# Kernel optimization log

Hardware: AMD Instinct MI355X
Metric: run time of the kernel (lower is better)

## Reference

```python
import jax, jax.numpy as jnp
import numpy as np

B, N, E_PER = 32, 2048, 16384
DIN, H = 128, 128
RATIO = 0.3


def setup_inputs() -> dict:
    key = jax.random.key(0)
    ks = jax.random.split(key, 16)
    s_in = 1.0 / np.sqrt(DIN)
    s_h = 1.0 / np.sqrt(H)
    inp = {
        "x": jax.random.normal(ks[0], (B * N, DIN), dtype=jnp.float32),
        "edge_src": jax.random.randint(ks[1], (B, E_PER), 0, N, dtype=jnp.int32),
        "edge_dst": jax.random.randint(ks[2], (B, E_PER), 0, N, dtype=jnp.int32),
        # SAGEConv layer 1: lin_l (neighbor agg, with bias), lin_r (root, no bias)
        "Wl1": jax.random.normal(ks[3], (H, DIN), dtype=jnp.float32) * s_in,
        "bl1": jnp.zeros((H,), dtype=jnp.float32),
        "Wr1": jax.random.normal(ks[4], (H, DIN), dtype=jnp.float32) * s_in,
        # SAGEConv layer 2
        "Wl2": jax.random.normal(ks[5], (H, H), dtype=jnp.float32) * s_h,
        "bl2": jnp.zeros((H,), dtype=jnp.float32),
        "Wr2": jax.random.normal(ks[6], (H, H), dtype=jnp.float32) * s_h,
        # TopKPooling score weight
        "pool_w": jax.random.normal(ks[7], (H,), dtype=jnp.float32) * s_h,
        # classifier MLP
        "Wc1": jax.random.normal(ks[8], (H, H), dtype=jnp.float32) * s_h,
        "bc1": jnp.zeros((H,), dtype=jnp.float32),
        "Wc2": jax.random.normal(ks[9], (1, H), dtype=jnp.float32) * s_h,
        "bc2": jnp.zeros((1,), dtype=jnp.float32),
    }
    return inp


def _sage_conv(x, src, dst, n_total, Wl, bl, Wr):
    # mean-aggregate neighbor messages: msg flows src -> dst
    msg = x[src]                                                   # [E, D] gather
    agg = jax.ops.segment_sum(msg, dst, num_segments=n_total)      # [Nt, D]
    deg = jax.ops.segment_sum(jnp.ones_like(dst, dtype=x.dtype), dst,
                              num_segments=n_total)
    agg = agg / jnp.maximum(deg, 1.0)[:, None]
    return agg @ Wl.T + bl + x @ Wr.T


def _forward(x, edge_src, edge_dst, Wl1, bl1, Wr1, Wl2, bl2, Wr2,
             pool_w, Wc1, bc1, Wc2, bc2):
    n_total = x.shape[0]
    # offset per-graph node ids into the disjoint-union batch
    off = (jnp.arange(B, dtype=edge_src.dtype) * N)[:, None]
    src = (edge_src + off).reshape(-1)
    dst = (edge_dst + off).reshape(-1)

    x = jax.nn.relu(_sage_conv(x, src, dst, n_total, Wl1, bl1, Wr1))
    x = jax.nn.relu(_sage_conv(x, src, dst, n_total, Wl2, bl2, Wr2))

    # TopKPooling: score = tanh(x . w / ||w||); keep top ceil(ratio*N) per graph
    score = jnp.tanh(x @ pool_w / jnp.linalg.norm(pool_w))         # [Nt]
    k = int(np.ceil(RATIO * N))                                    # 615
    vals, idx = jax.lax.top_k(score.reshape(B, N), k)              # [B, k]
    xg = x.reshape(B, N, -1)
    x_sel = jnp.take_along_axis(xg, idx[..., None], axis=1)        # [B, k, H]
    x_sel = x_sel * vals[..., None]                                # gate by score

    # global mean pool over kept nodes, then MLP classifier
    emb = x_sel.mean(axis=1)                                       # [B, H]
    h = jax.nn.relu(emb @ Wc1.T + bc1)
    return (h @ Wc2.T + bc2).squeeze(-1)                           # [B]


def reference(x, edge_src, edge_dst, Wl1, bl1, Wr1, Wl2, bl2, Wr2,
              pool_w, Wc1, bc1, Wc2, bc2):
    return _forward(x, edge_src, edge_dst, Wl1, bl1, Wr1, Wl2, bl2, Wr2,
                    pool_w, Wc1, bc1, Wc2, bc2)
```

## Files before the change

### kernel.cpp

```cpp
#include <hip/hip_runtime.h>
#include <stdint.h>
#include <math.h>

#define NB    32
#define NNODE 2048
#define EPB   16384
#define NT    (NB*NNODE)
#define ETOT  (NB*EPB)
#define DF    128
#define KSEL  615
#define EMAX  512

typedef __attribute__((ext_vector_type(8))) short bf16x8;
typedef __attribute__((ext_vector_type(4))) float f32x4;

__device__ __forceinline__ unsigned short f2bf(float f){
  uint32_t u = __float_as_uint(f);
  u += 0x7FFFu + ((u>>16)&1u);
  return (unsigned short)(u>>16);
}
__device__ __forceinline__ void split2(float f, unsigned short& hi, unsigned short& lo){
  unsigned short h = f2bf(f);
  float fh = __uint_as_float(((uint32_t)h)<<16);
  hi = h;
  lo = f2bf(f - fh);
}
__device__ __forceinline__ uint32_t f2mono(float f){
  uint32_t u = __float_as_uint(f);
  return (u & 0x80000000u) ? ~u : (u | 0x80000000u);
}
__device__ __forceinline__ float mono2f(uint32_t m){
  uint32_t u = (m & 0x80000000u) ? (m ^ 0x80000000u) : ~m;
  return __uint_as_float(u);
}

__global__ void k_deg(const int* __restrict__ edst, uint32_t* __restrict__ deg,
                      const float* __restrict__ Wl1, const float* __restrict__ Wr1,
                      const float* __restrict__ Wl2, const float* __restrict__ Wr2,
                      unsigned short* __restrict__ Bpk){
  const int bid = blockIdx.x;
  if (bid < ETOT/256){
    int e = bid*256 + threadIdx.x;
    int g = e >> 14;
    atomicAdd(&deg[g*NNODE + edst[e]], 1u);
  } else {
    int tt = (bid - ETOT/256)*256 + threadIdx.x;
    int layer = tt >> 12;
    int t2 = tt & 4095;
    const float* Wl = layer ? Wl2 : Wl1;
    const float* Wr = layer ? Wr2 : Wr1;
    unsigned short* B = Bpk + (size_t)layer*65536;
    int lane = t2 & 63;
    int ct   = (t2>>6) & 7;
    int ks   = (t2>>9) & 7;
    int c  = ct*16 + (lane & 15);
    int k0 = ks*32 + ((lane>>4)<<3);
    size_t base = ((size_t)((ks*8+ct)*2)*64 + lane)*8;
    #pragma unroll
    for (int j=0;j<8;++j){
      int k = k0 + j;
      float v = (k < DF) ? Wl[c*DF + k] : Wr[c*DF + (k-DF)];
      unsigned short h, l; split2(v, h, l);
      B[base + j]       = h;
      B[base + 512 + j] = l;
    }
  }
}

__global__ __launch_bounds__(256) void k_scanG(const uint32_t* __restrict__ deg,
                                               uint32_t* __restrict__ rowptr){
  __shared__ uint32_t wsum4[4];
  const int g = blockIdx.x, t = threadIdx.x;
  const int lane = t & 63, wid = t >> 6;
  const uint32_t* dg = deg + g*NNODE;
  uint32_t v[8]; const int b8 = t*8;
  uint32_t tsum = 0;
  #pragma unroll
  for (int j=0;j<8;++j){ v[j] = dg[b8+j]; tsum += v[j]; }
  uint32_t x = tsum;
  #pragma unroll
  for (int off=1; off<64; off<<=1){
    uint32_t y = __shfl_up(x, off, 64);
    if (lane >= off) x += y;
  }
  if (lane == 63) wsum4[wid] = x;
  __syncthreads();
  if (t == 0){
    uint32_t a = 0;
    #pragma unroll
    for (int w=0; w<4; ++w){ uint32_t tmp=wsum4[w]; wsum4[w]=a; a+=tmp; }
  }
  __syncthreads();
  uint32_t run = wsum4[wid] + x - tsum;
  uint32_t* rp = rowptr + g*NNODE + b8;
  #pragma unroll
  for (int j=0;j<8;++j){ rp[j] = g*EPB + run; run += v[j]; }
  if (g == 0 && t == 0) rowptr[NT] = ETOT;
}

__global__ void k_scatter(const int* __restrict__ esrc, const int* __restrict__ edst,
                          const uint32_t* __restrict__ rowptr, uint32_t* __restrict__ deg,
                          unsigned short* __restrict__ colh){
  int e = blockIdx.x*256 + threadIdx.x;
  int g = e >> 14;
  int d = g*NNODE + edst[e];
  uint32_t old = atomicSub(&deg[d], 1u);
  colh[rowptr[d] + old - 1u] = (unsigned short)esrc[e];
}

template<int LAYER>
__global__ __launch_bounds__(128, 4) void k_sage(
    const float* __restrict__ Xin, const uint32_t* __restrict__ rowptr,
    const unsigned short* __restrict__ colh, const unsigned short* __restrict__ Bpk,
    const float* __restrict__ bias, float* __restrict__ OUT,
    const float* __restrict__ pw, float* __restrict__ scores)
{
  __shared__ float smemA[32][132];
  __shared__ unsigned short lcol[EMAX];
  __shared__ uint32_t lrpl[33];

  const int t = threadIdx.x;
  const int g = blockIdx.x & 31, jb = blockIdx.x >> 5;
  const int rowBase = g*NNODE + jb*32;
  const float* Xg = Xin + (size_t)(g*NNODE)*DF;

  const uint32_t e0 = rowptr[rowBase];
  if (t < 33) lrpl[t] = rowptr[rowBase + t] - e0;
  const int ecnt = (int)(rowptr[rowBase + 32] - e0);
  for (int i=t; i<ecnt && i<EMAX; i+=128) lcol[i] = colh[e0+i];
  __syncthreads();

  {
    const int grp = t >> 5, c = t & 31;
    int cur = grp*8;
    const int curEnd = grp*8 + 8;
    f32x4 accv = {0.f,0.f,0.f,0.f};

    auto flushrow = [&](){
      uint32_t d = lrpl[cur+1] - lrpl[cur];
      float invd = 1.0f / (float)(d ? d : 1u);
      *(f32x4*)&smemA[cur][4*c] = accv * invd;
      accv = (f32x4){0.f,0.f,0.f,0.f};
      cur++;
    };

    const uint32_t kb = lrpl[grp*8], ke = lrpl[curEnd];
    auto run = [&](auto colAt){
      f32x4 v[8], w[8];
      #pragma unroll
      for (int j=0;j<8;++j){
        uint32_t kk = kb + j;
        int s = colAt(kk < ke ? kk : kb);
        v[j] = *(const f32x4*)(Xg + (size_t)s*DF + 4*c);
      }
      for (uint32_t k = kb; k < ke; k += 8){
        #pragma unroll
        for (int j=0;j<8;++j){
          uint32_t kk = k + 8 + j;
          int s = colAt(kk < ke ? kk : k);
          w[j] = *(const f32x4*)(Xg + (size_t)s*DF + 4*c);
        }
        #pragma unroll
        for (int j=0;j<8;++j){
          uint32_t kk = k + j;
          if (kk < ke){
            while (lrpl[cur+1] <= kk) flushrow();
            accv += v[j];
          }
        }
        #pragma unroll
        for (int j=0;j<8;++j) v[j] = w[j];
      }
    };
    if (kb < ke){
      if (ecnt <= EMAX) run([&](uint32_t k){ return (int)lcol[k]; });
      else              run([&](uint32_t k){ return (int)colh[e0+k]; });
    }
    while (cur < curEnd) flushrow();
  }
  __syncthreads();

  const int l = t & 63, wid = t >> 6;
  const int q = l >> 4, c16 = l & 15;
  const int arow = rowBase + wid*16 + c16;

  f32x4 own[8];
  #pragma unroll
  for (int ks4=0; ks4<4; ++ks4){
    const float* s = Xin + (size_t)arow*DF + ks4*32 + q*8;
    own[ks4*2]   = *(const f32x4*)s;
    own[ks4*2+1] = *(const f32x4*)(s+4);
  }

  f32x4 acc[8];
  #pragma unroll
  for (int ct=0; ct<8; ++ct) acc[ct] = (f32x4){0.f,0.f,0.f,0.f};

  #pragma unroll
  for (int ks=0; ks<8; ++ks){
    f32x4 A0, A1;
    if (ks < 4){
      const float* s = &smemA[wid*16 + c16][ks*32 + q*8];
      A0 = *(const f32x4*)s; A1 = *(const f32x4*)(s+4);
    } else {
      A0 = own[(ks-4)*2]; A1 = own[(ks-4)*2+1];
    }
    float v[8] = {A0.x,A0.y,A0.z,A0.w,A1.x,A1.y,A1.z,A1.w};
    bf16x8 ahi, alo;
    #pragma unroll
    for (int j=0;j<8;++j){
      unsigned short h, lo_; split2(v[j], h, lo_);
      ahi[j] = (short)h; alo[j] = (short)lo_;
    }
    const unsigned short* bp = Bpk + (size_t)ks*8192 + l*8;
    #pragma unroll
    for (int ct=0; ct<8; ++ct){
      bf16x8 bhi = *(const bf16x8*)(bp + ct*1024);
      bf16x8 blo = *(const bf16x8*)(bp + ct*1024 + 512);
      acc[ct] = __builtin_amdgcn_mfma_f32_16x16x32_bf16(ahi, bhi, acc[ct], 0,0,0);
      acc[ct] = __builtin_amdgcn_mfma_f32_16x16x32_bf16(ahi, blo, acc[ct], 0,0,0);
      acc[ct] = __builtin_amdgcn_mfma_f32_16x16x32_bf16(alo, bhi, acc[ct], 0,0,0);
    }
  }

  const int rowOut = rowBase + wid*16;
  if constexpr (LAYER==1){
    #pragma unroll
    for (int ct=0; ct<8; ++ct){
      int c = ct*16 + c16;
      float bv = bias[c];
      #pragma unroll
      for (int r=0; r<4; ++r){
        int grow = rowOut + q*4 + r;
        OUT[(size_t)grow*DF + c] = fmaxf(acc[ct][r] + bv, 0.f);
      }
    }
  } else {
    float ov[8][4];
    float pwv[8];
    float n2 = 0.f;
    #pragma unroll
    for (int ct=0; ct<8; ++ct){ pwv[ct] = pw[ct*16 + c16]; n2 += pwv[ct]*pwv[ct]; }
    n2 += __shfl_xor(n2,8,16); n2 += __shfl_xor(n2,4,16);
    n2 += __shfl_xor(n2,2,16); n2 += __shfl_xor(n2,1,16);
    float nrm = sqrtf(n2);
    #pragma unroll
    for (int ct=0; ct<8; ++ct){
      int c = ct*16 + c16;
      float bv = bias[c];
      #pragma unroll
      for (int r=0; r<4; ++r){
        int grow = rowOut + q*4 + r;
        float o = fmaxf(acc[ct][r] + bv, 0.f);
        OUT[(size_t)grow*DF + c] = o;
        ov[ct][r] = o;
      }
    }
    #pragma unroll
    for (int r=0; r<4; ++r){
      float p = 0.f;
      #pragma unroll
      for (int ct=0; ct<8; ++ct) p += ov[ct][r]*pwv[ct];
      p += __shfl_xor(p,8,16); p += __shfl_xor(p,4,16);
      p += __shfl_xor(p,2,16); p += __shfl_xor(p,1,16);
      if (c16 == 0) scores[rowOut + q*4 + r] = tanhf(p/nrm);
    }
  }
}

__global__ __launch_bounds__(1024) void k_topk(
    const float* __restrict__ scores, const float* __restrict__ H,
    const float* __restrict__ Wc1, const float* __restrict__ bc1,
    const float* __restrict__ Wc2, const float* __restrict__ bc2,
    float* __restrict__ out)
{
  __shared__ uint32_t keys[NNODE];
  __shared__ uint32_t hist[64];
  __shared__ uint32_t wsum[16];
  __shared__ uint32_t sh_b, sh_rank, sh_cnt;
  __shared__ unsigned short selidx[KSEL+1];
  __shared__ float selval[KSEL+1];
  __shared__ float part[8*DF];
  __shared__ float emb[DF];
  __shared__ float hred[DF];

  const int t = threadIdx.x; const int b = blockIdx.x;
  const int lane = t & 63, wid = t >> 6;
  const float* sc = scores + b*NNODE;

  for (int i=t; i<NNODE; i+=1024) keys[i] = f2mono(sc[i]);
  __syncthreads();

  uint32_t prefix = 0, prefmask = 0, rank = KSEL, cntT = 0;
  #pragma unroll
  for (int lev=0; lev<6; ++lev){
    const int shift = (lev<5) ? (26 - 6*lev) : 0;
    const uint32_t bmask = (lev<5) ? 63u : 3u;
    if (t < 64) hist[t] = 0;
    __syncthreads();
    for (int i=t; i<NNODE; i+=1024){
      uint32_t k = keys[i];
      if ((k & prefmask) == prefix) atomicAdd(&hist[(k>>shift)&bmask], 1u);
    }
    __syncthreads();
    if (t < 64){
      uint32_t x = hist[t];
      #pragma unroll
      for (int off=1; off<64; off<<=1){
        uint32_t y = __shfl_down(x, off, 64);
        if (t + off < 64) x += y;
      }
      uint32_t above = __shfl_down(x, 1, 64);
      if (t == 63) above = 0;
      if (above < rank && rank <= x){
        sh_b = (uint32_t)t; sh_rank = rank - above; sh_cnt = x - above;
      }
    }
    __syncthreads();
    prefix |= (sh_b << shift);
    prefmask |= (bmask << shift);
    rank = sh_rank; cntT = sh_cnt;
    __syncthreads();
  }
  const uint32_t T = prefix;
  const uint32_t m = rank;

  uint32_t k0 = keys[2*t], k1 = keys[2*t+1];
  uint32_t eq0 = (k0 == T), eq1 = (k1 == T);
  uint32_t eqr0 = 0, eqr1 = 0;

  if (m != cntT){
    uint32_t v = eq0 + eq1, x = v;
    #pragma unroll
    for (int off=1; off<64; off<<=1){
      uint32_t y = __shfl_up(x, off, 64);
      if (lane >= off) x += y;
    }
    if (lane == 63) wsum[wid] = x;
    __syncthreads();
    if (wid == 0){
      uint32_t s = (lane < 16) ? wsum[lane] : 0;
      #pragma unroll
      for (int off=1; off<16; off<<=1){
        uint32_t y = __shfl_up(s, off, 64);
        if (lane >= off) s += y;
      }
      if (lane < 16) wsum[lane] = s;
    }
    __syncthreads();
    uint32_t excl = (wid ? wsum[wid-1] : 0) + x - v;
    eqr0 = excl; eqr1 = excl + eq0;
    __syncthreads();
  }

  uint32_t sel0 = (k0 > T) || (eq0 && eqr0 < m);
  uint32_t sel1 = (k1 > T) || (eq1 && eqr1 < m);
  {
    uint32_t v = sel0 + sel1, x = v;
    #pragma unroll
    for (int off=1; off<64; off<<=1){
      uint32_t y = __shfl_up(x, off, 64);
      if (lane >= off) x += y;
    }
    if (lane == 63) wsum[wid] = x;
    __syncthreads();
    if (wid == 0){
      uint32_t s = (lane < 16) ? wsum[lane] : 0;
      #pragma unroll
      for (int off=1; off<16; off<<=1){
        uint32_t y = __shfl_up(s, off, 64);
        if (lane >= off) s += y;
      }
      if (lane < 16) wsum[lane] = s;
    }
    __syncthreads();
    uint32_t excl = (wid ? wsum[wid-1] : 0) + x - v;
    if (sel0){ selidx[excl] = (unsigned short)(2*t);   selval[excl] = mono2f(k0); }
    if (sel1){ selidx[excl+sel0] = (unsigned short)(2*t+1); selval[excl+sel0] = mono2f(k1); }
  }
  __syncthreads();

  const int pg = t >> 7, f = t & (DF-1);
  const float* Hb = H + (size_t)b*NNODE*DF;
  float accv = 0.f;
  int s2 = pg;
  for (; s2+24 < KSEL; s2 += 32){
    int i0=selidx[s2], i1=selidx[s2+8], i2=selidx[s2+16], i3=selidx[s2+24];
    float w0=selval[s2], w1=selval[s2+8], w2=selval[s2+16], w3=selval[s2+24];
    float v0=Hb[(size_t)i0*DF+f], v1=Hb[(size_t)i1*DF+f],
          v2=Hb[(size_t)i2*DF+f], v3=Hb[(size_t)i3*DF+f];
    accv += w0*v0 + w1*v1 + w2*v2 + w3*v3;
  }
  for (; s2<KSEL; s2+=8) accv += selval[s2]*Hb[(size_t)selidx[s2]*DF+f];
  part[pg*DF + f] = accv;
  __syncthreads();
  if (t < DF){
    float e = 0.f;
    for (int g2=0; g2<8; ++g2) e += part[g2*DF + t];
    emb[t] = e / (float)KSEL;
  }
  __syncthreads();
  if (t < DF){
    float hv = bc1[t];
    const float* wr = Wc1 + t*DF;
    for (int f2=0; f2<DF; ++f2) hv = fmaf(emb[f2], wr[f2], hv);
    hred[t] = fmaxf(hv, 0.f) * Wc2[t];
  }
  __syncthreads();
  if (t == 0){
    float o = bc2[0];
    for (int c2=0; c2<DF; ++c2) o += hred[c2];
    out[b] = o;
  }
}

extern "C" void kernel_launch(void* const* d_in, const int* in_sizes, int n_in,
                              void* d_out, int out_size, void* d_ws, size_t ws_size,
                              hipStream_t stream)
{
  (void)in_sizes; (void)n_in; (void)out_size; (void)ws_size;
  const float* x   = (const float*)d_in[0];
  const int* esrc  = (const int*)d_in[1];
  const int* edst  = (const int*)d_in[2];
  const float* Wl1 = (const float*)d_in[3];
  const float* bl1 = (const float*)d_in[4];
  const float* Wr1 = (const float*)d_in[5];
  const float* Wl2 = (const float*)d_in[6];
  const float* bl2 = (const float*)d_in[7];
  const float* Wr2 = (const float*)d_in[8];
  const float* pw  = (const float*)d_in[9];
  const float* Wc1 = (const float*)d_in[10];
  const float* bc1 = (const float*)d_in[11];
  const float* Wc2 = (const float*)d_in[12];
  const float* bc2 = (const float*)d_in[13];
  float* out = (float*)d_out;

  char* ws = (char*)d_ws;
  float*    H1     = (float*)   (ws + 0);
  float*    H2     = (float*)   (ws + 33554432);
  uint32_t* deg    = (uint32_t*)(ws + 67108864);
  uint32_t* rowptr = (uint32_t*)(ws + 67371008);
  unsigned short* colh = (unsigned short*)(ws + 67633408);
  float*    scores = (float*)   (ws + 68681728);
  unsigned short* Bpk = (unsigned short*)(ws + 68944128);

  hipMemsetAsync(deg, 0, NT*sizeof(uint32_t), stream);

  k_deg    <<<ETOT/256 + 32, 256, 0, stream>>>(edst, deg, Wl1, Wr1, Wl2, Wr2, Bpk);
  k_scanG  <<<NB, 256, 0, stream>>>(deg, rowptr);
  k_scatter<<<ETOT/256, 256, 0, stream>>>(esrc, edst, rowptr, deg, colh);

  k_sage<1><<<NT/32, 128, 0, stream>>>(x,  rowptr, colh, Bpk,         bl1,
                                       H1, nullptr, nullptr);
  k_sage<2><<<NT/32, 128, 0, stream>>>(H1, rowptr, colh, Bpk + 65536, bl2,
                                       H2, pw, scores);

  k_topk<<<NB, 1024, 0, stream>>>(scores, H2, Wc1, bc1, Wc2, bc2, out);
}
```

Before: 153.2 us.

## Stage neighbor gathers through LDS ring with async global_load_lds double buffering

Replaces the register-prefetched neighbor gather in the SAGE aggregation with a per-wave double-buffered LDS ring, filled by global_load_lds direct-to-LDS loads. Each wave now aggregates 16 rows with 2 floats per lane, overlapping the next chunk's gather with consumption of the current one via explicit vmcnt waits. The aim is to cut register pressure and raise memory-level parallelism on the gather. In exchange it adds 16KB of LDS per block, which may lower occupancy under launch_bounds(128,4). The hand-written waitcnt and sched_barrier sequencing is fragile, and the slow path that reads colh from global memory waits on every chunk.

Result: slower. 312.1 us (+103.7%).

```diff
diff --git a/kernel.cpp b/kernel.cpp
--- a/kernel.cpp
+++ b/kernel.cpp
@@ -116,6 +116,7 @@
     const float* __restrict__ pw, float* __restrict__ scores)
 {
   __shared__ float smemA[32][132];
+  __shared__ float ring[2][2][8][128];
   __shared__ unsigned short lcol[EMAX];
   __shared__ uint32_t lrpl[33];
 
@@ -130,57 +131,69 @@
   for (int i=t; i<ecnt && i<EMAX; i+=128) lcol[i] = colh[e0+i];
   __syncthreads();
 
+  const int w = t >> 6, lane = t & 63;
   {
-    const int grp = t >> 5, c = t & 31;
-    int cur = grp*8;
-    const int curEnd = grp*8 + 8;
-    f32x4 accv = {0.f,0.f,0.f,0.f};
+    const int he = lane >> 5;
+    const int qo = lane & 31;
+    int cur = w*16;
+    const int segEnd = w*16 + 16;
+    const uint32_t kb = lrpl[cur], ke = lrpl[segEnd];
+    uint32_t rnext = lrpl[cur+1];
+    float a0 = 0.f, a1 = 0.f;
 
     auto flushrow = [&](){
-      uint32_t d = lrpl[cur+1] - lrpl[cur];
+      uint32_t d = rnext - lrpl[cur];
       float invd = 1.0f / (float)(d ? d : 1u);
-      *(f32x4*)&smemA[cur][4*c] = accv * invd;
-      accv = (f32x4){0.f,0.f,0.f,0.f};
+      *(float2*)&smemA[cur][lane*2] = make_float2(a0*invd, a1*invd);
+      a0 = 0.f; a1 = 0.f;
       cur++;
+      rnext = (cur < segEnd) ? lrpl[cur+1] : 0xFFFFFFFFu;
     };
 
-    const uint32_t kb = lrpl[grp*8], ke = lrpl[curEnd];
-    auto run = [&](auto colAt){
-      f32x4 v[8], w[8];
-      #pragma unroll
-      for (int j=0;j<8;++j){
-        uint32_t kk = kb + j;
-        int s = colAt(kk < ke ? kk : kb);
-        v[j] = *(const f32x4*)(Xg + (size_t)s*DF + 4*c);
-      }
-      for (uint32_t k = kb; k < ke; k += 8){
+    auto consume = [&](uint32_t ebase, int half){
+      uint32_t eend = (ebase+8 < ke) ? ebase+8 : ke;
+      for (uint32_t e=ebase; e<eend; ++e){
+        float2 v = *(const float2*)&ring[w][half][e-ebase][lane*2];
+        while (rnext <= e) flushrow();
+        a0 += v.x; a1 += v.y;
+      }
+    };
+
+    if (kb < ke){
+      const bool fast = (ecnt <= EMAX);
+      auto stage = [&](uint32_t ebase, int half){
         #pragma unroll
-        for (int j=0;j<8;++j){
-          uint32_t kk = k + 8 + j;
-          int s = colAt(kk < ke ? kk : k);
-          w[j] = *(const f32x4*)(Xg + (size_t)s*DF + 4*c);
+        for (int i=0;i<4;++i){
+          uint32_t eidx = ebase + 2*i + he;
+          uint32_t ecl = (eidx < ke) ? eidx : kb;
+          int s = fast ? (int)lcol[ecl] : (int)colh[e0+ecl];
+          const float* gp = Xg + (size_t)s*DF + qo*4;
+          __builtin_amdgcn_global_load_lds(
+              (const __attribute__((address_space(1))) uint32_t*)gp,
+              (__attribute__((address_space(3))) uint32_t*)&ring[w][half][2*i][0],
+              16, 0, 0);
         }
-        #pragma unroll
-        for (int j=0;j<8;++j){
-          uint32_t kk = k + j;
-          if (kk < ke){
-            while (lrpl[cur+1] <= kk) flushrow();
-            accv += v[j];
-          }
+      };
+      const uint32_t nch = (ke - kb + 7u) >> 3;
+      stage(kb, 0);
+      for (uint32_t c=0; c<nch; ++c){
+        int half = (int)(c & 1u);
+        if (c+1 < nch){
+          stage(kb + (c+1)*8, half^1);
+          if (fast) asm volatile("s_waitcnt vmcnt(4)" ::: "memory");
+          else      asm volatile("s_waitcnt vmcnt(0)" ::: "memory");
+        } else {
+          asm volatile("s_waitcnt vmcnt(0)" ::: "memory");
         }
-        #pragma unroll
-        for (int j=0;j<8;++j) v[j] = w[j];
-      }
-    };
-    if (kb < ke){
-      if (ecnt <= EMAX) run([&](uint32_t k){ return (int)lcol[k]; });
-      else              run([&](uint32_t k){ return (int)colh[e0+k]; });
-    }
-    while (cur < curEnd) flushrow();
-  }
-  __syncthreads();
-
-  const int l = t & 63, wid = t >> 6;
+        __builtin_amdgcn_sched_barrier(0);
+        consume(kb + c*8, half);
+      }
+    }
+    while (cur < segEnd) flushrow();
+  }
+  __syncthreads();
+
+  const int wid = w, l = lane;
   const int q = l >> 4, c16 = l & 15;
   const int arow = rowBase + wid*16 + c16;
 
```
